# Performance work log

Hardware: AMD Instinct MI355X
Metric: run time of the kernel (lower is better)

## Reference

```python
import jax, jax.numpy as jnp
import numpy as np

N = 50000       # population nodes
E = 1_600_000   # edges per edge type
F_IN = 2000     # flattened individual-graph embedding (100*20)
D = 20          # hidden channels per TransformerConv head (heads=1)
NEG_SLOPE = 0.01
BN_EPS = 1e-5


def setup_inputs() -> dict:
    key = jax.random.key(0)
    ks = jax.random.split(key, 24)
    features = jax.random.normal(ks[0], (N, F_IN), jnp.float32)
    same_index = jax.random.randint(ks[1], (2, E), 0, N, dtype=jnp.int64)
    diff_index = jax.random.randint(ks[2], (2, E), 0, N, dtype=jnp.int64)
    s0 = 1.0 / np.sqrt(F_IN)
    s1 = 1.0 / np.sqrt(D)
    # layer 0 conv params, stacked over the 2 edge types (same, diff)
    W0q = jax.random.normal(ks[3], (2, F_IN, D), jnp.float32) * s0
    W0k = jax.random.normal(ks[4], (2, F_IN, D), jnp.float32) * s0
    W0v = jax.random.normal(ks[5], (2, F_IN, D), jnp.float32) * s0
    W0s = jax.random.normal(ks[6], (2, F_IN, D), jnp.float32) * s0
    b0q = jnp.zeros((2, D)); b0k = jnp.zeros((2, D))
    b0v = jnp.zeros((2, D)); b0s = jnp.zeros((2, D))
    # layers 1..3 conv params: [layer, edge_type, D, D]
    Wq = jax.random.normal(ks[7], (3, 2, D, D), jnp.float32) * s1
    Wk = jax.random.normal(ks[8], (3, 2, D, D), jnp.float32) * s1
    Wv = jax.random.normal(ks[9], (3, 2, D, D), jnp.float32) * s1
    Ws = jax.random.normal(ks[10], (3, 2, D, D), jnp.float32) * s1
    bq = jnp.zeros((3, 2, D)); bk = jnp.zeros((3, 2, D))
    bv = jnp.zeros((3, 2, D)); bs = jnp.zeros((3, 2, D))
    w1 = jnp.full((4,), 0.8, jnp.float32)
    w2 = jnp.full((4,), 0.2, jnp.float32)
    bn_gamma = jnp.ones((4, D), jnp.float32)
    bn_beta = jnp.zeros((4, D), jnp.float32)
    Wout = jax.random.normal(ks[11], (4 * D, 2), jnp.float32) / np.sqrt(4 * D)
    bout = jnp.zeros((2,), jnp.float32)
    return dict(features=features, same_index=same_index, diff_index=diff_index,
                W0q=W0q, b0q=b0q, W0k=W0k, b0k=b0k, W0v=W0v, b0v=b0v, W0s=W0s, b0s=b0s,
                Wq=Wq, bq=bq, Wk=Wk, bk=bk, Wv=Wv, bv=bv, Ws=Ws, bs=bs,
                w1=w1, w2=w2, bn_gamma=bn_gamma, bn_beta=bn_beta, Wout=Wout, bout=bout)


def _tconv(x, edge_index, Wq, bq, Wk, bk, Wv, bv, Ws, bs):
    """PyG TransformerConv, heads=1, concat=True, root_weight=True, no edge_attr."""
    src, dst = edge_index[0], edge_index[1]
    q = x @ Wq + bq   # [N, D]
    k = x @ Wk + bk
    v = x @ Wv + bv
    logits = jnp.einsum('ed,ed->e', q[dst], k[src]) / jnp.sqrt(jnp.float32(D))  # [E]
    m = jax.ops.segment_max(logits, dst, num_segments=N)
    m = jnp.where(jnp.isfinite(m), m, jnp.float32(0.0))  # nodes with no in-edges
    e = jnp.exp(logits - m[dst])
    z = jax.ops.segment_sum(e, dst, num_segments=N)
    alpha = e / (z[dst] + 1e-16)  # PyG softmax epsilon
    agg = jax.ops.segment_sum(alpha[:, None] * v[src], dst, num_segments=N)  # [N, D]
    return agg + x @ Ws + bs  # skip (root) connection


def _bn(x, gamma, beta):
    mu = x.mean(axis=0)
    var = x.var(axis=0)
    return (x - mu) * jax.lax.rsqrt(var + BN_EPS) * gamma + beta


def reference(features, same_index, diff_index,
              W0q, b0q, W0k, b0k, W0v, b0v, W0s, b0s,
              Wq, bq, Wk, bk, Wv, bv, Ws, bs,
              w1, w2, bn_gamma, bn_beta, Wout, bout):
    x = features
    fcs = []
    for l in range(4):
        if l == 0:
            p_same = (W0q[0], b0q[0], W0k[0], b0k[0], W0v[0], b0v[0], W0s[0], b0s[0])
            p_diff = (W0q[1], b0q[1], W0k[1], b0k[1], W0v[1], b0v[1], W0s[1], b0s[1])
        else:
            i = l - 1
            p_same = (Wq[i, 0], bq[i, 0], Wk[i, 0], bk[i, 0], Wv[i, 0], bv[i, 0], Ws[i, 0], bs[i, 0])
            p_diff = (Wq[i, 1], bq[i, 1], Wk[i, 1], bk[i, 1], Wv[i, 1], bv[i, 1], Ws[i, 1], bs[i, 1])
        x1 = _tconv(x, same_index, *p_same)
        x2 = _tconv(x, diff_index, *p_diff)
        t = w1[l] + w2[l]
        x = (w1[l] / t) * x1 + (w2[l] / t) * x2
        x = _bn(x, bn_gamma[l], bn_beta[l])
        x = jax.nn.leaky_relu(x, NEG_SLOPE)
        fcs.append(x)
    fc = jnp.concatenate(fcs, axis=-1)  # [N, 80]
    return fc @ Wout + bout  # [N, 2]
```

## Files before the change

### kernel.cpp

```cpp
#include <hip/hip_runtime.h>
#include <math.h>

#define N_NODES 50000
#define E_EDGES 1600000
#define F_IN    2000
#define D       20
#define NCOL    160
#define KPAD    2016
#define NBNP    64
#define LSTR    40

#define INV_SQRT_D 0.22360679774997896f

typedef __bf16 bf16x8 __attribute__((ext_vector_type(8)));
typedef __bf16 bf16x4 __attribute__((ext_vector_type(4)));
typedef float  f32x4  __attribute__((ext_vector_type(4)));


__global__ void pack_kernel(
    const float* __restrict__ W0q, const float* __restrict__ W0k,
    const float* __restrict__ W0v, const float* __restrict__ W0s,
    const float* __restrict__ b0q, const float* __restrict__ b0k,
    const float* __restrict__ b0v, const float* __restrict__ b0s,
    const float* __restrict__ Wq,  const float* __restrict__ Wk,
    const float* __restrict__ Wv,  const float* __restrict__ Ws_,
    const float* __restrict__ bq,  const float* __restrict__ bk,
    const float* __restrict__ bv,  const float* __restrict__ bs_,
    __bf16* __restrict__ B0, float* __restrict__ bias0,
    float* __restrict__ WL, float* __restrict__ biasL,
    float* __restrict__ bnp, int* __restrict__ deg)
{
  long idx = (long)blockIdx.x * blockDim.x + threadIdx.x;
  if (idx < (long)NCOL*KPAD) {
    int col = (int)(idx / KPAD), k = (int)(idx % KPAD);
    int et = col / 80, r = col % 80, mat = r / 20, d = r % 20;
    const float* w = (mat==0)?W0q:(mat==1)?W0s:(mat==2)?W0k:W0v;
    float v = (k < F_IN) ? w[((size_t)et*F_IN + k)*D + d] : 0.f;
    B0[idx] = (__bf16)v;
    return;
  }
  idx -= (long)NCOL*KPAD;
  if (idx < 160) {
    int col = (int)idx;
    int et = col / 80, r = col % 80, mat = r / 20, d = r % 20;
    const float* b = (mat==0)?b0q:(mat==1)?b0s:(mat==2)?b0k:b0v;
    bias0[col] = b[et*D + d];
    return;
  }
  idx -= 160;
  if (idx < 9600) {
    int l = (int)(idx / 3200), rem = (int)(idx % 3200);
    int k = rem / NCOL, col = rem % NCOL;
    int et = col / 80, r = col % 80, mat = r / 20, d = r % 20;
    const float* w = (mat==0)?Wq:(mat==1)?Ws_:(mat==2)?Wk:Wv;
    WL[idx] = w[(((size_t)l*2 + et)*D + k)*D + d];
    return;
  }
  idx -= 9600;
  if (idx < 480) {
    int l = (int)(idx / NCOL), col = (int)(idx % NCOL);
    int et = col / 80, r = col % 80, mat = r / 20, d = r % 20;
    const float* b = (mat==0)?bq:(mat==1)?bs_:(mat==2)?bk:bv;
    biasL[idx] = b[(l*2 + et)*D + d];
    return;
  }
  idx -= 480;
  if (idx < 4*NBNP*40) { bnp[idx] = 0.f; return; }
  idx -= 4*NBNP*40;
  if (idx < 2*N_NODES) { deg[idx] = 0; return; }
}

#define SC_EPT 16
#define SC_CHUNK (256*SC_EPT)

__global__ void hist_kernel(const int* __restrict__ same, const int* __restrict__ diff,
                            int* __restrict__ deg)
{
  const int part  = blockIdx.x & 7;
  const int chunk = blockIdx.x >> 3;
  const int lo = part * (N_NODES/8);
  const int hi = lo + (N_NODES/8);
  const long i0 = (long)chunk * SC_CHUNK + threadIdx.x;
#pragma unroll
  for (int it = 0; it < SC_EPT; ++it) {
    long i = i0 + (long)it*256;
    if (i >= 2L*E_EDGES) break;
    int et = (i >= E_EDGES) ? 1 : 0;
    long e = i - (long)et*E_EDGES;
    const int* ix = et ? diff : same;
    int dst = ix[E_EDGES + e];
    if (dst >= lo && dst < hi)
      atomicAdd(&deg[(size_t)et*N_NODES + dst], 1);
  }
}

__global__ void scan_kernel(const int* __restrict__ deg,
                            int* __restrict__ rowptr0, int* __restrict__ rowptr1,
                            int* __restrict__ next0, int* __restrict__ next1)
{
  const int et = blockIdx.x;
  const int* dg = deg + (size_t)et*N_NODES;
  int* rp = et ? rowptr1 : rowptr0;
  int* np = et ? next1 : next0;
  __shared__ int part[1024];
  const int t = threadIdx.x;
  const int per = (N_NODES + 1023) / 1024;
  const int b = t * per;
  const int e = (b + per < N_NODES) ? (b + per) : N_NODES;
  int s = 0;
  for (int i = b; i < e; i++) s += dg[i];
  part[t] = s;
  __syncthreads();
  for (int o = 1; o < 1024; o <<= 1) {
    int v = (t >= o) ? part[t-o] : 0;
    __syncthreads();
    part[t] += v;
    __syncthreads();
  }
  int run = (t == 0) ? 0 : part[t-1];
  for (int i = b; i < e; i++) {
    rp[i] = run; np[i] = run;
    run += dg[i];
  }
  if (t == 0) rp[N_NODES] = part[1023];
}

__global__ void scatter_kernel(const int* __restrict__ same, const int* __restrict__ diff,
                               int* __restrict__ next0, int* __restrict__ next1,
                               int* __restrict__ adj0, int* __restrict__ adj1)
{
  const int part  = blockIdx.x & 7;
  const int chunk = blockIdx.x >> 3;
  const int lo = part * (N_NODES/8);
  const int hi = lo + (N_NODES/8);
  const long i0 = (long)chunk * SC_CHUNK + threadIdx.x;
#pragma unroll
  for (int it = 0; it < SC_EPT; ++it) {
    long i = i0 + (long)it*256;
    if (i >= 2L*E_EDGES) break;
    int et = (i >= E_EDGES) ? 1 : 0;
    long e = i - (long)et*E_EDGES;
    const int* ix = et ? diff : same;
    int dst = ix[E_EDGES + e];
    if (dst >= lo && dst < hi) {
      int src = ix[e];
      int* np  = et ? next1 : next0;
      int* adj = et ? adj1  : adj0;
      int pos = atomicAdd(&np[dst], 1);
      adj[pos] = src;
    }
  }
}

__launch_bounds__(128)
__global__ void gemm0_mfma(const float* __restrict__ A,
                           const __bf16* __restrict__ Bt,
                           const float* __restrict__ bias,
                           __bf16* __restrict__ QS,
                           __bf16* __restrict__ KV0, __bf16* __restrict__ KV1)
{
  __shared__ __bf16 as[2][32*LSTR];
  const int t    = threadIdx.x;
  const int lane = t & 63;
  const int wc   = t >> 6;
  const int rb0  = blockIdx.x * 32;

  const int srow = t >> 2;
  const int skc  = (t & 3) * 8;
  const int arow = rb0 + srow;
  const float* aptr = A + (size_t)arow * F_IN;

  const int lrow = lane & 15;
  const int lkb  = (lane >> 4) * 8;

  f32x4 acc[2][5];
#pragma unroll
  for (int i = 0; i < 2; i++)
#pragma unroll
    for (int j = 0; j < 5; j++) acc[i][j] = (f32x4){0.f,0.f,0.f,0.f};

  auto loadA = [&](int s, float4& q0, float4& q1) {
    int k = s*32 + skc;
    if (arow < N_NODES && k + 8 <= F_IN) {
      q0 = *(const float4*)(aptr + k);
      q1 = *(const float4*)(aptr + k + 4);
    } else {
      q0 = make_float4(0,0,0,0); q1 = q0;
    }
  };
  auto cvtStore = [&](int buf, const float4& q0, const float4& q1) {
    bf16x8 h;
    h[0]=(__bf16)q0.x; h[1]=(__bf16)q0.y; h[2]=(__bf16)q0.z; h[3]=(__bf16)q0.w;
    h[4]=(__bf16)q1.x; h[5]=(__bf16)q1.y; h[6]=(__bf16)q1.z; h[7]=(__bf16)q1.w;
    *(bf16x8*)&as[buf][srow*LSTR + skc] = h;
  };

  float4 pa0, pa1, pb0, pb1;
  loadA(0,  pa0, pa1);
  loadA(1,  pb0, pb1);
  cvtStore(0, pa0, pa1);
  __syncthreads();

  for (int s = 0; s < 63; s++) {
    const int cur = s & 1;
    bf16x8 af[2];
#pragma unroll
    for (int rf = 0; rf < 2; rf++)
      af[rf] = *(bf16x8*)&as[cur][(rf*16 + lrow)*LSTR + lkb];
    bf16x8 bfr[5];
#pragma unroll
    for (int cf = 0; cf < 5; cf++)
      bfr[cf] = *(const bf16x8*)(Bt + (size_t)(wc*80 + cf*16 + lrow)*KPAD + s*32 + lkb);

    if (s + 1 < 63) cvtStore(cur ^ 1, pb0, pb1);
    if (s + 2 < 63) loadA((s + 2), pa0, pa1);

#pragma unroll
    for (int rf = 0; rf < 2; rf++)
#pragma unroll
      for (int cf = 0; cf < 5; cf++)
        acc[rf][cf] = __builtin_amdgcn_mfma_f32_16x16x32_bf16(af[rf], bfr[cf], acc[rf][cf], 0, 0, 0);
    __syncthreads();

    float4 t0 = pa0, t1 = pa1;
    pa0 = pb0; pa1 = pb1;
    pb0 = t0;  pb1 = t1;
  }

#pragma unroll
  for (int rf = 0; rf < 2; rf++) {
#pragma unroll
    for (int cf = 0; cf < 5; cf++) {
      int col = wc*80 + cf*16 + lrow;
      int et = col / 80, r = col % 80, mat = r / 20, d = r % 20;
      float bv = bias[col];
      __bf16* kvp = et ? KV1 : KV0;
#pragma unroll
      for (int j = 0; j < 4; j++) {
        int row = rb0 + rf*16 + (lane >> 4)*4 + j;
        if (row < N_NODES) {
          __bf16 val = (__bf16)(acc[rf][cf][j] + bv);
          if (mat < 2) QS[(size_t)row*80 + et*40 + mat*20 + d] = val;
          else         kvp[(size_t)row*64 + (mat-2)*20 + d]   = val;
        }
      }
    }
  }
}

__launch_bounds__(256)
__global__ void proj_small_kernel(const float* __restrict__ xp, const float* __restrict__ bnl,
                                  const float* __restrict__ gam, const float* __restrict__ bet,
                                  const float* __restrict__ W, const float* __restrict__ bias,
                                  __bf16* __restrict__ QS,
                                  __bf16* __restrict__ KV0, __bf16* __restrict__ KV1)
{
  __shared__ float ws[20*160];
  __shared__ float xs[16*20];
  __shared__ float Ac[20], Bc[20];
  const int t = threadIdx.x;
  const int n0 = blockIdx.x * 16;
#pragma unroll
  for (int i = 0; i < 13; i++) {
    int idx = t + i*256;
    if (idx < 3200) ws[idx] = W[idx];
  }
  if (t < 20) {
    float s1 = 0.f, s2 = 0.f;
    for (int s = 0; s < NBNP; s++) { s1 += bnl[s*40 + t]; s2 += bnl[s*40 + 20 + t]; }
    float mu  = s1 * (1.f/N_NODES);
    float var = s2 * (1.f/N_NODES) - mu*mu;
    float a = rsqrtf(var + 1e-5f) * gam[t];
    Ac[t] = a; Bc[t] = bet[t] - mu*a;
  }
  __syncthreads();
#pragma unroll
  for (int i = 0; i < 2; i++) {
    int idx = t + i*256;
    if (idx < 320) {
      int nl = idx / 20, k = idx % 20;
      int n = n0 + nl;
      float x = (n < N_NODES) ? xp[(size_t)n*D + k] : 0.f;
      float y = x*Ac[k] + Bc[k];
      xs[idx] = (y > 0.f) ? y : 0.01f*y;
    }
  }
  __syncthreads();
#pragma unroll
  for (int i = 0; i < 10; i++) {
    int idx = t + i*256;
    int nl = idx / NCOL, col = idx % NCOL;
    int n = n0 + nl;
    if (n < N_NODES) {
      float acc = bias[col];
#pragma unroll
      for (int k = 0; k < 20; k++) acc += xs[nl*20 + k] * ws[k*NCOL + col];
      int et = col / 80, r = col % 80, mat = r / 20, d = r % 20;
      __bf16 val = (__bf16)acc;
      if (mat < 2) QS[(size_t)n*80 + et*40 + mat*20 + d] = val;
      else         (et ? KV1 : KV0)[(size_t)n*64 + (mat-2)*20 + d] = val;
    }
  }
}

__launch_bounds__(256)
__global__ void attn_fused(const int* __restrict__ rp0, const int* __restrict__ adj0,
                           const int* __restrict__ rp1, const int* __restrict__ adj1,
                           const __bf16* __restrict__ QS,
                           const __bf16* __restrict__ KV0, const __bf16* __restrict__ KV1,
                           const float* __restrict__ w1, const float* __restrict__ w2, int l,
                           float* __restrict__ xpre, float* __restrict__ bnp)
{
  const int t    = threadIdx.x;
  const int wv   = t >> 6;
  const int lane = t & 63;
  const int g    = lane >> 4;
  const int sl   = lane & 15;
  const int et   = g & 1;
  const int node = blockIdx.x*8 + wv*2 + (g >> 1);

  const int* rowptr = et ? rp1 : rp0;
  const int* adj    = et ? adj1 : adj0;
  const __bf16* kvb = et ? KV1 : KV0;
  const __bf16* rq  = QS + (size_t)node*80 + et*40;

  float qf[20];
  {
    bf16x8 q0 = *(const bf16x8*)(rq);
    bf16x8 q1 = *(const bf16x8*)(rq + 8);
    bf16x4 q2 = *(const bf16x4*)(rq + 16);
#pragma unroll
    for (int i = 0; i < 8; i++) { qf[i] = (float)q0[i]; qf[8+i] = (float)q1[i]; }
#pragma unroll
    for (int i = 0; i < 4; i++) qf[16+i] = (float)q2[i];
  }

  const int beg = rowptr[node], end = rowptr[node+1];
  float z = 0.f;
  float S[20];
#pragma unroll
  for (int d = 0; d < 20; d++) S[d] = 0.f;

  int i = beg + sl;
  for (; i + 16 < end; i += 32) {
    const int s0 = adj[i], s1 = adj[i+16];
    const __bf16* kva = kvb + (size_t)s0*64;
    const __bf16* kvc = kvb + (size_t)s1*64;
    bf16x8 a0 = *(const bf16x8*)(kva);
    bf16x8 a1 = *(const bf16x8*)(kva + 8);
    bf16x8 a2 = *(const bf16x8*)(kva + 16);
    bf16x8 a3 = *(const bf16x8*)(kva + 24);
    bf16x8 a4 = *(const bf16x8*)(kva + 32);
    bf16x8 b0 = *(const bf16x8*)(kvc);
    bf16x8 b1 = *(const bf16x8*)(kvc + 8);
    bf16x8 b2 = *(const bf16x8*)(kvc + 16);
    bf16x8 b3 = *(const bf16x8*)(kvc + 24);
    bf16x8 b4 = *(const bf16x8*)(kvc + 32);

    float d0 = 0.f, d1 = 0.f;
#pragma unroll
    for (int j = 0; j < 8; j++) { d0 += qf[j]*(float)a0[j];     d1 += qf[j]*(float)b0[j]; }
#pragma unroll
    for (int j = 0; j < 8; j++) { d0 += qf[8+j]*(float)a1[j];   d1 += qf[8+j]*(float)b1[j]; }
#pragma unroll
    for (int j = 0; j < 4; j++) { d0 += qf[16+j]*(float)a2[j];  d1 += qf[16+j]*(float)b2[j]; }
    const float w0 = __expf(fminf(d0*INV_SQRT_D, 80.f));
    const float w1v= __expf(fminf(d1*INV_SQRT_D, 80.f));
    z += w0 + w1v;
#pragma unroll
    for (int d = 0; d < 4; d++) S[d]     += w0*(float)a2[4+d] + w1v*(float)b2[4+d];
#pragma unroll
    for (int d = 0; d < 8; d++) S[4+d]   += w0*(float)a3[d]   + w1v*(float)b3[d];
#pragma unroll
    for (int d = 0; d < 8; d++) S[12+d]  += w0*(float)a4[d]   + w1v*(float)b4[d];
  }
  if (i < end) {
    const int s0 = adj[i];
    const __bf16* kva = kvb + (size_t)s0*64;
    bf16x8 a0 = *(const bf16x8*)(kva);
    bf16x8 a1 = *(const bf16x8*)(kva + 8);
    bf16x8 a2 = *(const bf16x8*)(kva + 16);
    bf16x8 a3 = *(const bf16x8*)(kva + 24);
    bf16x8 a4 = *(const bf16x8*)(kva + 32);
    float d0 = 0.f;
#pragma unroll
    for (int j = 0; j < 8; j++) d0 += qf[j]     * (float)a0[j];
#pragma unroll
    for (int j = 0; j < 8; j++) d0 += qf[8 + j] * (float)a1[j];
#pragma unroll
    for (int j = 0; j < 4; j++) d0 += qf[16 + j]* (float)a2[j];
    const float w0 = __expf(fminf(d0*INV_SQRT_D, 80.f));
    z += w0;
#pragma unroll
    for (int d = 0; d < 4; d++) S[d]     += w0*(float)a2[4+d];
#pragma unroll
    for (int d = 0; d < 8; d++) S[4+d]   += w0*(float)a3[d];
#pragma unroll
    for (int d = 0; d < 8; d++) S[12+d]  += w0*(float)a4[d];
  }

#pragma unroll
  for (int o = 8; o >= 1; o >>= 1) {
    z += __shfl_xor(z, o, 64);
#pragma unroll
    for (int d = 0; d < 20; d++) S[d] += __shfl_xor(S[d], o, 64);
  }

  const float inv = (z > 0.f) ? 1.f/z : 0.f;
  float outv[20];
  {
    bf16x4 s0 = *(const bf16x4*)(rq + 20);
    bf16x8 s1 = *(const bf16x8*)(rq + 24);
    bf16x8 s2 = *(const bf16x8*)(rq + 32);
#pragma unroll
    for (int i2 = 0; i2 < 4; i2++) outv[i2] = S[i2]*inv + (float)s0[i2];
#pragma unroll
    for (int i2 = 0; i2 < 8; i2++) { outv[4+i2]  = S[4+i2]*inv  + (float)s1[i2];
                                     outv[12+i2] = S[12+i2]*inv + (float)s2[i2]; }
  }

  const float wa = w1[l], wb = w2[l];
  const float c0 = wa/(wa+wb), c1 = wb/(wa+wb);
  const float cme = et ? c1 : c0;
  const float cot = et ? c0 : c1;
  float x[20];
#pragma unroll
  for (int d = 0; d < 20; d++) {
    float o2 = __shfl_xor(outv[d], 16, 64);
    x[d] = cme*outv[d] + cot*o2;
  }

  if (et == 0 && sl == 0) {
    float* xo = xpre + (size_t)node*D;
#pragma unroll
    for (int j = 0; j < 5; j++) {
      float4 o4 = make_float4(x[4*j], x[4*j+1], x[4*j+2], x[4*j+3]);
      *(float4*)(xo + 4*j) = o4;
    }
  }

  float v = x[0];
#pragma unroll
  for (int d = 1; d < 16; d++) v = (sl == d) ? x[d] : v;
  float v2 = x[16];
#pragma unroll
  for (int d = 1; d < 4; d++) v2 = (sl == d) ? x[16 + d] : v2;

  float* slot = bnp + (size_t)(node & (NBNP-1))*40;
  if (et == 0) {
    atomicAdd(&slot[sl], v);
    if (sl < 4) atomicAdd(&slot[16 + sl], v2);
  } else {
    atomicAdd(&slot[20 + sl], v*v);
    if (sl < 4) atomicAdd(&slot[36 + sl], v2*v2);
  }
}

__launch_bounds__(256)
__global__ void final_kernel(const float* __restrict__ xpre4, const float* __restrict__ bnp,
                             const float* __restrict__ gam, const float* __restrict__ bet,
                             const float* __restrict__ Wout, const float* __restrict__ bout,
                             float* __restrict__ out)
{
  __shared__ float Ac[80], Bc[80], wlds[160];
  const int t = threadIdx.x;
  if (t < 80) {
    int l = t / 20, d = t % 20;
    const float* b = bnp + l*(NBNP*40);
    float s1 = 0.f, s2 = 0.f;
    for (int s = 0; s < NBNP; s++) { s1 += b[s*40 + d]; s2 += b[s*40 + 20 + d]; }
    float mu  = s1 * (1.f/N_NODES);
    float var = s2 * (1.f/N_NODES) - mu*mu;
    float a = rsqrtf(var + 1e-5f) * gam[t];
    Ac[t] = a; Bc[t] = bet[t] - mu*a;
  }
  if (t < 160) wlds[t] = Wout[t];
  __syncthreads();

  const int n = blockIdx.x*256 + t;
  if (n >= N_NODES) return;
  float a0 = bout[0], a1 = bout[1];
#pragma unroll
  for (int l = 0; l < 4; l++) {
    const float* base = xpre4 + (size_t)l*N_NODES*D + (size_t)n*D;
#pragma unroll
    for (int d = 0; d < D; d++) {
      int idx = l*20 + d;
      float y = base[d]*Ac[idx] + Bc[idx];
      y = (y > 0.f) ? y : 0.01f*y;
      a0 += y * wlds[idx*2 + 0];
      a1 += y * wlds[idx*2 + 1];
    }
  }
  out[n*2+0] = a0;
  out[n*2+1] = a1;
}

extern "C" void kernel_launch(void* const* d_in, const int* in_sizes, int n_in,
                              void* d_out, int out_size, void* d_ws, size_t ws_size,
                              hipStream_t stream)
{
  const float* feat = (const float*)d_in[0];
  const int*   same = (const int*)d_in[1];
  const int*   diff = (const int*)d_in[2];
  const float* W0q = (const float*)d_in[3];
  const float* b0q = (const float*)d_in[4];
  const float* W0k = (const float*)d_in[5];
  const float* b0k = (const float*)d_in[6];
  const float* W0v = (const float*)d_in[7];
  const float* b0v = (const float*)d_in[8];
  const float* W0s = (const float*)d_in[9];
  const float* b0s = (const float*)d_in[10];
  const float* Wq  = (const float*)d_in[11];
  const float* bq  = (const float*)d_in[12];
  const float* Wk  = (const float*)d_in[13];
  const float* bk  = (const float*)d_in[14];
  const float* Wv  = (const float*)d_in[15];
  const float* bv  = (const float*)d_in[16];
  const float* Ws_ = (const float*)d_in[17];
  const float* bs_ = (const float*)d_in[18];
  const float* w1  = (const float*)d_in[19];
  const float* w2  = (const float*)d_in[20];
  const float* gamma = (const float*)d_in[21];
  const float* beta  = (const float*)d_in[22];
  const float* Wout  = (const float*)d_in[23];
  const float* bout  = (const float*)d_in[24];

  float* wsf  = (float*)d_ws;
  __bf16*  QS    = (__bf16*)wsf;
  __bf16*  KV0   = (__bf16*)(wsf + 2000000);
  __bf16*  KV1   = (__bf16*)(wsf + 3600000);
  float*   XPRE4 = wsf + 5200000;
  __bf16*  B0bf  = (__bf16*)(wsf + 9200000);
  float*   BIAS0 = wsf + 9361280;
  float*   WL    = wsf + 9361440;
  float*   BIASL = wsf + 9371040;
  float*   BNP   = wsf + 9371520;
  int*     ib    = (int*)(wsf + 9381760);
  int* DEG  = ib;
  int* RP0  = ib + 100000;
  int* RP1  = ib + 150004;
  int* NX0  = ib + 200008;
  int* NX1  = ib + 250008;
  int* ADJ0 = ib + 300008;
  int* ADJ1 = ib + 1900008;

  const int packN = NCOL*KPAD + 160 + 9600 + 480 + 4*NBNP*40 + 2*N_NODES;
  pack_kernel<<<(packN + 255)/256, 256, 0, stream>>>(
      W0q, W0k, W0v, W0s, b0q, b0k, b0v, b0s,
      Wq, Wk, Wv, Ws_, bq, bk, bv, bs_,
      B0bf, BIAS0, WL, BIASL, BNP, DEG);

  const long nchunk = (2L*E_EDGES + SC_CHUNK - 1) / SC_CHUNK;
  hist_kernel<<<(int)(nchunk*8), 256, 0, stream>>>(same, diff, DEG);
  scan_kernel<<<2, 1024, 0, stream>>>(DEG, RP0, RP1, NX0, NX1);
  scatter_kernel<<<(int)(nchunk*8), 256, 0, stream>>>(same, diff, NX0, NX1, ADJ0, ADJ1);

  for (int l = 0; l < 4; l++) {
    if (l == 0)
      gemm0_mfma<<<(N_NODES + 31)/32, 128, 0, stream>>>(feat, B0bf, BIAS0, QS, KV0, KV1);
    else
      proj_small_kernel<<<(N_NODES + 15)/16, 256, 0, stream>>>(
          XPRE4 + (size_t)(l-1)*N_NODES*D, BNP + (l-1)*(NBNP*40),
          gamma + (l-1)*D, beta + (l-1)*D,
          WL + (size_t)(l-1)*3200, BIASL + (size_t)(l-1)*160, QS, KV0, KV1);

    attn_fused<<<N_NODES/8, 256, 0, stream>>>(
        RP0, ADJ0, RP1, ADJ1, QS, KV0, KV1, w1, w2, l,
        XPRE4 + (size_t)l*N_NODES*D, BNP + l*(NBNP*40));
  }

  final_kernel<<<(N_NODES + 255)/256, 256, 0, stream>>>(
      XPRE4, BNP, gamma, beta, Wout, bout, (float*)d_out);
}
```

Baseline: 1.095 ms.

## Split-K layer-0 GEMM and co-launch it with histogram and scatter kernels

The layer-0 feature GEMM is split into two K halves on 64-row tiles with four waves per block. Its blocks share a launch with the degree-histogram blocks, and the partial sums are combined with the bias in a second kernel that also hosts the CSR scatter. This is meant to give the GEMM more parallelism and to overlap the atomic-bound graph construction with compute. In exchange it writes and reads two fp32 partial buffers of N×160 elements, which adds memory traffic.

```diff
diff --git a/kernel.cpp b/kernel.cpp
--- a/kernel.cpp
+++ b/kernel.cpp
@@ -6,7 +6,9 @@
 #define F_IN    2000
 #define D       20
 #define NCOL    160
-#define KPAD    2016
+#define KPAD2   2048
+#define KHALF   1024
+#define KSTEPS  32
 #define NBNP    64
 #define LSTR    40
 
@@ -31,15 +33,15 @@
     float* __restrict__ bnp, int* __restrict__ deg)
 {
   long idx = (long)blockIdx.x * blockDim.x + threadIdx.x;
-  if (idx < (long)NCOL*KPAD) {
-    int col = (int)(idx / KPAD), k = (int)(idx % KPAD);
+  if (idx < (long)NCOL*KPAD2) {
+    int col = (int)(idx / KPAD2), k = (int)(idx % KPAD2);
     int et = col / 80, r = col % 80, mat = r / 20, d = r % 20;
     const float* w = (mat==0)?W0q:(mat==1)?W0s:(mat==2)?W0k:W0v;
     float v = (k < F_IN) ? w[((size_t)et*F_IN + k)*D + d] : 0.f;
     B0[idx] = (__bf16)v;
     return;
   }
-  idx -= (long)NCOL*KPAD;
+  idx -= (long)NCOL*KPAD2;
   if (idx < 160) {
     int col = (int)idx;
     int et = col / 80, r = col % 80, mat = r / 20, d = r % 20;
@@ -72,27 +74,6 @@
 
 #define SC_EPT 16
 #define SC_CHUNK (256*SC_EPT)
-
-__global__ void hist_kernel(const int* __restrict__ same, const int* __restrict__ diff,
-                            int* __restrict__ deg)
-{
-  const int part  = blockIdx.x & 7;
-  const int chunk = blockIdx.x >> 3;
-  const int lo = part * (N_NODES/8);
-  const int hi = lo + (N_NODES/8);
-  const long i0 = (long)chunk * SC_CHUNK + threadIdx.x;
-#pragma unroll
-  for (int it = 0; it < SC_EPT; ++it) {
-    long i = i0 + (long)it*256;
-    if (i >= 2L*E_EDGES) break;
-    int et = (i >= E_EDGES) ? 1 : 0;
-    long e = i - (long)et*E_EDGES;
-    const int* ix = et ? diff : same;
-    int dst = ix[E_EDGES + e];
-    if (dst >= lo && dst < hi)
-      atomicAdd(&deg[(size_t)et*N_NODES + dst], 1);
-  }
-}
 
 __global__ void scan_kernel(const int* __restrict__ deg,
                             int* __restrict__ rowptr0, int* __restrict__ rowptr1,
@@ -125,45 +106,43 @@
   if (t == 0) rp[N_NODES] = part[1023];
 }
 
-__global__ void scatter_kernel(const int* __restrict__ same, const int* __restrict__ diff,
-                               int* __restrict__ next0, int* __restrict__ next1,
-                               int* __restrict__ adj0, int* __restrict__ adj1)
-{
-  const int part  = blockIdx.x & 7;
-  const int chunk = blockIdx.x >> 3;
-  const int lo = part * (N_NODES/8);
-  const int hi = lo + (N_NODES/8);
-  const long i0 = (long)chunk * SC_CHUNK + threadIdx.x;
-#pragma unroll
-  for (int it = 0; it < SC_EPT; ++it) {
-    long i = i0 + (long)it*256;
-    if (i >= 2L*E_EDGES) break;
-    int et = (i >= E_EDGES) ? 1 : 0;
-    long e = i - (long)et*E_EDGES;
-    const int* ix = et ? diff : same;
-    int dst = ix[E_EDGES + e];
-    if (dst >= lo && dst < hi) {
-      int src = ix[e];
-      int* np  = et ? next1 : next0;
-      int* adj = et ? adj1  : adj0;
-      int pos = atomicAdd(&np[dst], 1);
-      adj[pos] = src;
-    }
-  }
-}
-
-__launch_bounds__(128)
-__global__ void gemm0_mfma(const float* __restrict__ A,
-                           const __bf16* __restrict__ Bt,
-                           const float* __restrict__ bias,
-                           __bf16* __restrict__ QS,
-                           __bf16* __restrict__ KV0, __bf16* __restrict__ KV1)
-{
-  __shared__ __bf16 as[2][32*LSTR];
+__launch_bounds__(256)
+__global__ void k1_gemm0_hist(const float* __restrict__ A,
+                              const __bf16* __restrict__ Bt,
+                              float* __restrict__ CP,
+                              const int* __restrict__ same, const int* __restrict__ diff,
+                              int* __restrict__ deg, int gemmBlocks)
+{
+  if ((int)blockIdx.x >= gemmBlocks) {
+    const int bid   = blockIdx.x - gemmBlocks;
+    const int part  = bid & 7;
+    const int chunk = bid >> 3;
+    const int lo = part * (N_NODES/8);
+    const int hi = lo + (N_NODES/8);
+    const long i0 = (long)chunk * SC_CHUNK + threadIdx.x;
+#pragma unroll
+    for (int it = 0; it < SC_EPT; ++it) {
+      long i = i0 + (long)it*256;
+      if (i >= 2L*E_EDGES) break;
+      int et = (i >= E_EDGES) ? 1 : 0;
+      long e = i - (long)et*E_EDGES;
+      const int* ix = et ? diff : same;
+      int dst = ix[E_EDGES + e];
+      if (dst >= lo && dst < hi)
+        atomicAdd(&deg[(size_t)et*N_NODES + dst], 1);
+    }
+    return;
+  }
+
+  __shared__ __bf16 as[2][64*LSTR];
+  const int tile = blockIdx.x >> 1;
+  const int kh   = blockIdx.x & 1;
   const int t    = threadIdx.x;
   const int lane = t & 63;
-  const int wc   = t >> 6;
-  const int rb0  = blockIdx.x * 32;
+  const int wid  = t >> 6;
+  const int wr   = wid >> 1;
+  const int wc   = wid & 1;
+  const int rb0  = tile * 64;
 
   const int srow = t >> 2;
   const int skc  = (t & 3) * 8;
@@ -180,7 +159,7 @@
     for (int j = 0; j < 5; j++) acc[i][j] = (f32x4){0.f,0.f,0.f,0.f};
 
   auto loadA = [&](int s, float4& q0, float4& q1) {
-    int k = s*32 + skc;
+    int k = kh*KHALF + s*32 + skc;
     if (arow < N_NODES && k + 8 <= F_IN) {
       q0 = *(const float4*)(aptr + k);
       q1 = *(const float4*)(aptr + k + 4);
@@ -196,24 +175,24 @@
   };
 
   float4 pa0, pa1, pb0, pb1;
-  loadA(0,  pa0, pa1);
-  loadA(1,  pb0, pb1);
+  loadA(0, pa0, pa1);
+  loadA(1, pb0, pb1);
   cvtStore(0, pa0, pa1);
   __syncthreads();
 
-  for (int s = 0; s < 63; s++) {
+  for (int s = 0; s < KSTEPS; s++) {
     const int cur = s & 1;
     bf16x8 af[2];
 #pragma unroll
     for (int rf = 0; rf < 2; rf++)
-      af[rf] = *(bf16x8*)&as[cur][(rf*16 + lrow)*LSTR + lkb];
+      af[rf] = *(bf16x8*)&as[cur][(wr*32 + rf*16 + lrow)*LSTR + lkb];
     bf16x8 bfr[5];
 #pragma unroll
     for (int cf = 0; cf < 5; cf++)
-      bfr[cf] = *(const bf16x8*)(Bt + (size_t)(wc*80 + cf*16 + lrow)*KPAD + s*32 + lkb);
-
-    if (s + 1 < 63) cvtStore(cur ^ 1, pb0, pb1);
-    if (s + 2 < 63) loadA((s + 2), pa0, pa1);
+      bfr[cf] = *(const bf16x8*)(Bt + (size_t)(wc*80 + cf*16 + lrow)*KPAD2 + kh*KHALF + s*32 + lkb);
+
+    if (s + 1 < KSTEPS) cvtStore(cur ^ 1, pb0, pb1);
+    if (s + 2 < KSTEPS) loadA(s + 2, pa0, pa1);
 
 #pragma unroll
     for (int rf = 0; rf < 2; rf++)
@@ -227,24 +206,74 @@
     pb0 = t0;  pb1 = t1;
   }
 
+  float* cp = CP + (size_t)kh*N_NODES*NCOL;
 #pragma unroll
   for (int rf = 0; rf < 2; rf++) {
 #pragma unroll
     for (int cf = 0; cf < 5; cf++) {
       int col = wc*80 + cf*16 + lrow;
-      int et = col / 80, r = col % 80, mat = r / 20, d = r % 20;
-      float bv = bias[col];
-      __bf16* kvp = et ? KV1 : KV0;
 #pragma unroll
       for (int j = 0; j < 4; j++) {
-        int row = rb0 + rf*16 + (lane >> 4)*4 + j;
-        if (row < N_NODES) {
-          __bf16 val = (__bf16)(acc[rf][cf][j] + bv);
-          if (mat < 2) QS[(size_t)row*80 + et*40 + mat*20 + d] = val;
-          else         kvp[(size_t)row*64 + (mat-2)*20 + d]   = val;
-        }
+        int row = rb0 + wr*32 + rf*16 + (lane >> 4)*4 + j;
+        if (row < N_NODES) cp[(size_t)row*NCOL + col] = acc[rf][cf][j];
       }
     }
+  }
+}
+
+__launch_bounds__(256)
+__global__ void k2_combine_scatter(const float* __restrict__ CP, const float* __restrict__ bias,
+                                   __bf16* __restrict__ QS,
+                                   __bf16* __restrict__ KV0, __bf16* __restrict__ KV1,
+                                   const int* __restrict__ same, const int* __restrict__ diff,
+                                   int* __restrict__ next0, int* __restrict__ next1,
+                                   int* __restrict__ adj0, int* __restrict__ adj1,
+                                   int combBlocks)
+{
+  if ((int)blockIdx.x >= combBlocks) {
+    const int bid   = blockIdx.x - combBlocks;
+    const int part  = bid & 7;
+    const int chunk = bid >> 3;
+    const int lo = part * (N_NODES/8);
+    const int hi = lo + (N_NODES/8);
+    const long i0 = (long)chunk * SC_CHUNK + threadIdx.x;
+#pragma unroll
+    for (int it = 0; it < SC_EPT; ++it) {
+      long i = i0 + (long)it*256;
+      if (i >= 2L*E_EDGES) break;
+      int et = (i >= E_EDGES) ? 1 : 0;
+      long e = i - (long)et*E_EDGES;
+      const int* ix = et ? diff : same;
+      int dst = ix[E_EDGES + e];
+      if (dst >= lo && dst < hi) {
+        int src = ix[e];
+        int* np  = et ? next1 : next0;
+        int* adj = et ? adj1  : adj0;
+        int pos = atomicAdd(&np[dst], 1);
+        adj[pos] = src;
+      }
+    }
+    return;
+  }
+
+  const long base = ((long)blockIdx.x*256 + threadIdx.x) * 4;
+  if (base >= (long)N_NODES*NCOL) return;
+  const int row = (int)(base / NCOL);
+  const int col = (int)(base % NCOL);
+  float4 a = *(const float4*)(CP + base);
+  float4 b = *(const float4*)(CP + (size_t)N_NODES*NCOL + base);
+  float4 bi = *(const float4*)(bias + col);
+  float v[4] = { a.x+b.x+bi.x, a.y+b.y+bi.y, a.z+b.z+bi.z, a.w+b.w+bi.w };
+
+  const int et = col / 80, r = col % 80, mat = r / 20, d = r % 20;
+  if (mat < 2) {
+    __bf16* q = QS + (size_t)row*80 + et*40 + mat*20 + d;
+#pragma unroll
+    for (int j = 0; j < 4; j++) q[j] = (__bf16)v[j];
+  } else {
+    __bf16* kv = (et ? KV1 : KV0) + (size_t)row*64 + (mat-2)*20 + d;
+#pragma unroll
+    for (int j = 0; j < 4; j++) kv[j] = (__bf16)v[j];
   }
 }
 
@@ -532,11 +561,12 @@
   __bf16*  KV1   = (__bf16*)(wsf + 3600000);
   float*   XPRE4 = wsf + 5200000;
   __bf16*  B0bf  = (__bf16*)(wsf + 9200000);
-  float*   BIAS0 = wsf + 9361280;
-  float*   WL    = wsf + 9361440;
-  float*   BIASL = wsf + 9371040;
-  float*   BNP   = wsf + 9371520;
-  int*     ib    = (int*)(wsf + 9381760);
+  float*   BIAS0 = wsf + 9363840;
+  float*   WL    = wsf + 9364000;
+  float*   BIASL = wsf + 9373600;
+  float*   BNP   = wsf + 9374080;
+  float*   CP    = wsf + 9400000;
+  int*     ib    = (int*)(wsf + 25400000);
   int* DEG  = ib;
   int* RP0  = ib + 100000;
   int* RP1  = ib + 150004;
@@ -545,21 +575,27 @@
   int* ADJ0 = ib + 300008;
   int* ADJ1 = ib + 1900008;
 
-  const int packN = NCOL*KPAD + 160 + 9600 + 480 + 4*NBNP*40 + 2*N_NODES;
+  const int packN = NCOL*KPAD2 + 160 + 9600 + 480 + 4*NBNP*40 + 2*N_NODES;
   pack_kernel<<<(packN + 255)/256, 256, 0, stream>>>(
       W0q, W0k, W0v, W0s, b0q, b0k, b0v, b0s,
       Wq, Wk, Wv, Ws_, bq, bk, bv, bs_,
       B0bf, BIAS0, WL, BIASL, BNP, DEG);
 
   const long nchunk = (2L*E_EDGES + SC_CHUNK - 1) / SC_CHUNK;
-  hist_kernel<<<(int)(nchunk*8), 256, 0, stream>>>(same, diff, DEG);
+  const int histBlocks = (int)(nchunk*8);
+  const int gemmBlocks = ((N_NODES + 63)/64) * 2;
+  const int combBlocks = (int)(((long)N_NODES*NCOL/4 + 255) / 256);
+
+  k1_gemm0_hist<<<gemmBlocks + histBlocks, 256, 0, stream>>>(
+      feat, B0bf, CP, same, diff, DEG, gemmBlocks);
+
   scan_kernel<<<2, 1024, 0, stream>>>(DEG, RP0, RP1, NX0, NX1);
-  scatter_kernel<<<(int)(nchunk*8), 256, 0, stream>>>(same, diff, NX0, NX1, ADJ0, ADJ1);
+
+  k2_combine_scatter<<<combBlocks + histBlocks, 256, 0, stream>>>(
+      CP, BIAS0, QS, KV0, KV1, same, diff, NX0, NX1, ADJ0, ADJ1, combBlocks);
 
   for (int l = 0; l < 4; l++) {
-    if (l == 0)
-      gemm0_mfma<<<(N_NODES + 31)/32, 128, 0, stream>>>(feat, B0bf, BIAS0, QS, KV0, KV1);
-    else
+    if (l > 0)
       proj_small_kernel<<<(N_NODES + 15)/16, 256, 0, stream>>>(
           XPRE4 + (size_t)(l-1)*N_NODES*D, BNP + (l-1)*(NBNP*40),
           gamma + (l-1)*D, beta + (l-1)*D,
```

Result: faster. 1.019 ms (-7.0%).
